# Kernel optimization log

Measured on AMD Instinct MI355X. Metric: run time of the kernel, lower is better.

## Reference

```python
import jax, jax.numpy as jnp
import numpy as np

B = 131072
UNITS = 256
INPUT_DIM = 256


def setup_inputs() -> dict:
    key = jax.random.key(0)
    ks = jax.random.split(key, 8)
    x = jax.random.normal(ks[0], (B, INPUT_DIM), dtype=jnp.float32)
    h_prev = jax.random.normal(ks[1], (B, UNITS), dtype=jnp.float32)
    c_prev = jax.random.normal(ks[2], (B, UNITS), dtype=jnp.float32)
    # glorot-like scale for W: fan_in = INPUT_DIM + UNITS, fan_out = 4*UNITS
    scale = jnp.sqrt(2.0 / (INPUT_DIM + UNITS + 4 * UNITS)).astype(jnp.float32)
    W = jax.random.normal(ks[3], (INPUT_DIM + UNITS, 4 * UNITS), dtype=jnp.float32) * scale
    # bias: zeros except forget gate initialized to 1.0
    b = jnp.concatenate([
        jnp.zeros(UNITS, jnp.float32),
        jnp.ones(UNITS, jnp.float32),
        jnp.zeros(UNITS, jnp.float32),
        jnp.zeros(UNITS, jnp.float32),
    ])
    peephole_i = jax.random.normal(ks[4], (UNITS,), dtype=jnp.float32) * 0.05
    peephole_f = jax.random.normal(ks[5], (UNITS,), dtype=jnp.float32) * 0.05
    peephole_o = jax.random.normal(ks[6], (UNITS,), dtype=jnp.float32) * 0.05
    return {
        "x": x, "h_prev": h_prev, "c_prev": c_prev,
        "W": W, "b": b,
        "peephole_i": peephole_i, "peephole_f": peephole_f, "peephole_o": peephole_o,
    }


def reference(x, h_prev, c_prev, W, b, peephole_i, peephole_f, peephole_o):
    combined = jnp.concatenate([x, h_prev], axis=-1)          # [B, INPUT_DIM+UNITS]
    z = combined @ W + b                                      # [B, 4*UNITS]
    i, f, c_hat, o = jnp.split(z, 4, axis=1)                  # each [B, UNITS]
    i = jax.nn.sigmoid(i + peephole_i * c_prev)
    f = jax.nn.sigmoid(f + peephole_f * c_prev)
    o = jax.nn.sigmoid(o + peephole_o * c_prev)
    c_hat = jnp.tanh(c_hat)
    c = f * c_prev + i * c_hat
    h = o * jnp.tanh(c)
    return (h, h, c)  # matches (output, [h, c]) of the Keras cell
```

## Files before the change

### kernel.cpp

```cpp
#include <hip/hip_runtime.h>
#include <hip/hip_bf16.h>
#include <cstdint>

#define NROWS   131072
#define NUNITS  256
#define N4      1024
#define KTOT    512
#define BM      64
#define THREADS 512

typedef float f32x4 __attribute__((ext_vector_type(4)));
typedef short bf16x8 __attribute__((ext_vector_type(8)));

__device__ __forceinline__ short f2bf(float x) {
    unsigned u = __float_as_uint(x);
    u += 0x7FFFu + ((u >> 16) & 1u);
    return (short)(u >> 16);
}

__global__ void convert_W_kernel(const float* __restrict__ W, short* __restrict__ Wws) {
    int i = blockIdx.x * 256 + threadIdx.x;
    int k = i >> 10;
    int c = i & 1023;
    short b = f2bf(W[i]);
    Wws[((size_t)(k >> 5) << 15) + ((size_t)c << 5) + (k & 31)] = b;
}

__global__ void __launch_bounds__(THREADS, 4)
lstm_main_kernel(const float* __restrict__ x, const float* __restrict__ h_prev,
                 const float* __restrict__ c_prev, const float* __restrict__ bias,
                 const float* __restrict__ pi, const float* __restrict__ pf,
                 const float* __restrict__ po, const short* __restrict__ Wws,
                 float* __restrict__ out) {
    __shared__ short Alds[2][BM * 32];

    const int t    = threadIdx.x;
    const int lane = t & 63;
    const int w    = t >> 6;
    const int rt   = blockIdx.x >> 1;
    const int ch   = blockIdx.x & 1;
    const int row0 = rt * BM;

    const int lr = lane & 15;
    const int hi = lane >> 4;

    const int srow = t >> 3;
    const int sh   = t & 7;
    const int sg   = sh >> 1;
    const int shalf= sh & 1;
    const int s_lds = srow * 32 + ((sg ^ ((srow >> 1) & 3)) * 8) + shalf * 4;
    const float* aRowX = x      + (size_t)(row0 + srow) * 256 + sh * 4;
    const float* aRowH = h_prev + (size_t)(row0 + srow) * 256 + sh * 4;

    const int a_rd = lr * 32 + ((hi ^ ((lr >> 1) & 3)) * 8);

    const int ucol = ch * 128 + w * 16 + lr;
    const short* wbase = Wws + (size_t)ucol * 32 + hi * 8;

    f32x4 acc[4][4];
    #pragma unroll
    for (int m = 0; m < 4; ++m)
        #pragma unroll
        for (int g = 0; g < 4; ++g)
            acc[m][g] = (f32x4){0.f, 0.f, 0.f, 0.f};

    auto stage = [&](int kidx, int buf) {
        const float* src = (kidx < 8 ? aRowX : aRowH) + (kidx & 7) * 32;
        float4 av = *(const float4*)src;
        unsigned p0 = ((unsigned)(unsigned short)f2bf(av.y) << 16) | (unsigned short)f2bf(av.x);
        unsigned p1 = ((unsigned)(unsigned short)f2bf(av.w) << 16) | (unsigned short)f2bf(av.z);
        *(uint2*)(&Alds[buf][s_lds]) = make_uint2(p0, p1);
    };

    auto compute = [&](int ks, int buf) {
        const short* wk = wbase + ((size_t)ks << 15);
        bf16x8 bf[4];
        #pragma unroll
        for (int g = 0; g < 4; ++g)
            bf[g] = *(const bf16x8*)(wk + g * 8192);
        bf16x8 af[4];
        #pragma unroll
        for (int m = 0; m < 4; ++m)
            af[m] = *(const bf16x8*)&Alds[buf][a_rd + m * 16 * 32];
        #pragma unroll
        for (int g = 0; g < 4; ++g)
            #pragma unroll
            for (int m = 0; m < 4; ++m)
                acc[m][g] = __builtin_amdgcn_mfma_f32_16x16x32_bf16(af[m], bf[g], acc[m][g], 0, 0, 0);
    };

    stage(0, 0);
    __syncthreads();

    #pragma unroll 1
    for (int ks2 = 0; ks2 < 8; ++ks2) {
        const int k0 = ks2 * 2;
        stage(k0 + 1, 1);
        compute(k0, 0);
        __syncthreads();
        if (ks2 < 7) stage(k0 + 2, 0);
        compute(k0 + 1, 1);
        __syncthreads();
    }

    const size_t HS = (size_t)NROWS * NUNITS;
    const int u = ucol;
    const float bi = bias[u],       bfg = bias[256 + u];
    const float bc = bias[512 + u], bo  = bias[768 + u];
    const float ppi = pi[u], ppf = pf[u], ppo = po[u];
    #pragma unroll
    for (int m = 0; m < 4; ++m) {
        #pragma unroll
        for (int r = 0; r < 4; ++r) {
            const int row = row0 + m * 16 + hi * 4 + r;
            const size_t o = (size_t)row * NUNITS + u;
            const float cp = c_prev[o];
            float zi = acc[m][0][r] + bi  + ppi * cp;
            float zf = acc[m][1][r] + bfg + ppf * cp;
            float zc = acc[m][2][r] + bc;
            float zo = acc[m][3][r] + bo  + ppo * cp;
            float ig = 1.f / (1.f + __expf(-zi));
            float fg = 1.f / (1.f + __expf(-zf));
            float og = 1.f / (1.f + __expf(-zo));
            zc = fminf(fmaxf(zc, -30.f), 30.f);
            float e2 = __expf(2.f * zc);
            float chat = (e2 - 1.f) / (e2 + 1.f);
            float c  = fg * cp + ig * chat;
            float ccl = fminf(fmaxf(c, -30.f), 30.f);
            float e3 = __expf(2.f * ccl);
            float th = (e3 - 1.f) / (e3 + 1.f);
            float h  = og * th;
            out[o]          = h;
            out[HS + o]     = h;
            out[2 * HS + o] = c;
        }
    }
}

extern "C" void kernel_launch(void* const* d_in, const int* in_sizes, int n_in,
                              void* d_out, int out_size, void* d_ws, size_t ws_size,
                              hipStream_t stream) {
    const float* x  = (const float*)d_in[0];
    const float* h  = (const float*)d_in[1];
    const float* c  = (const float*)d_in[2];
    const float* W  = (const float*)d_in[3];
    const float* b  = (const float*)d_in[4];
    const float* pi = (const float*)d_in[5];
    const float* pf = (const float*)d_in[6];
    const float* po = (const float*)d_in[7];
    short* Wws = (short*)d_ws;
    float* out = (float*)d_out;

    hipLaunchKernelGGL(convert_W_kernel, dim3(2048), dim3(256), 0, stream, W, Wws);
    hipLaunchKernelGGL(lstm_main_kernel, dim3(2 * NROWS / BM), dim3(THREADS), 0, stream,
                       x, h, c, b, pi, pf, po, Wws, out);
}
```

Baseline: 334.5 us.

## Switch to 32x32 MFMA, drop LDS staging, pre-convert activations to bf16

Replaces the 16x16x32 MFMA tiling with 32x32x16 MFMAs. Each wave now owns a 32-row by 32-unit tile per gate and reads A fragments directly from global memory, so the LDS double buffer and the barriers are gone. When the workspace is large enough, a separate kernel first converts x and h_prev into a bf16 concatenated matrix, which halves the A read traffic in the main kernel but adds an extra pass that writes and rereads 128MB. The W workspace layout changes to 16-k chunks to match the new MFMA shape.

```diff
diff --git a/kernel.cpp b/kernel.cpp
--- a/kernel.cpp
+++ b/kernel.cpp
@@ -4,12 +4,12 @@
 
 #define NROWS   131072
 #define NUNITS  256
-#define N4      1024
 #define KTOT    512
 #define BM      64
 #define THREADS 512
 
-typedef float f32x4 __attribute__((ext_vector_type(4)));
+typedef float f32x16 __attribute__((ext_vector_type(16)));
+typedef float f32x4  __attribute__((ext_vector_type(4)));
 typedef short bf16x8 __attribute__((ext_vector_type(8)));
 
 __device__ __forceinline__ short f2bf(float x) {
@@ -22,118 +22,112 @@
     int i = blockIdx.x * 256 + threadIdx.x;
     int k = i >> 10;
     int c = i & 1023;
-    short b = f2bf(W[i]);
-    Wws[((size_t)(k >> 5) << 15) + ((size_t)c << 5) + (k & 31)] = b;
+    Wws[((size_t)(k >> 4) << 14) + ((size_t)c << 4) + (k & 15)] = f2bf(W[i]);
 }
 
+__global__ void convert_A_kernel(const float* __restrict__ x, const float* __restrict__ h,
+                                 short* __restrict__ Aws) {
+    int i = blockIdx.x * 256 + threadIdx.x;
+    int row = i >> 6;
+    int c   = (i & 63) * 4;
+    float4 xv = *(const float4*)(x + (size_t)row * 256 + c);
+    float4 hv = *(const float4*)(h + (size_t)row * 256 + c);
+    short xs[4] = {f2bf(xv.x), f2bf(xv.y), f2bf(xv.z), f2bf(xv.w)};
+    short hs[4] = {f2bf(hv.x), f2bf(hv.y), f2bf(hv.z), f2bf(hv.w)};
+    *(uint2*)(Aws + (size_t)row * 512 + c)       = *(uint2*)xs;
+    *(uint2*)(Aws + (size_t)row * 512 + 256 + c) = *(uint2*)hs;
+}
+
+template<bool PRE>
 __global__ void __launch_bounds__(THREADS, 4)
 lstm_main_kernel(const float* __restrict__ x, const float* __restrict__ h_prev,
                  const float* __restrict__ c_prev, const float* __restrict__ bias,
                  const float* __restrict__ pi, const float* __restrict__ pf,
                  const float* __restrict__ po, const short* __restrict__ Wws,
-                 float* __restrict__ out) {
-    __shared__ short Alds[2][BM * 32];
-
+                 const short* __restrict__ Aws, float* __restrict__ out) {
     const int t    = threadIdx.x;
     const int lane = t & 63;
     const int w    = t >> 6;
+    const int mg   = w >> 2;
+    const int cs   = w & 3;
     const int rt   = blockIdx.x >> 1;
     const int ch   = blockIdx.x & 1;
-    const int row0 = rt * BM;
+    const int l5   = lane & 31;
+    const int k8   = lane >> 5;
 
-    const int lr = lane & 15;
-    const int hi = lane >> 4;
+    const int row  = rt * BM + mg * 32 + l5;
+    const int u    = ch * 128 + cs * 32 + l5;
 
-    const int srow = t >> 3;
-    const int sh   = t & 7;
-    const int sg   = sh >> 1;
-    const int shalf= sh & 1;
-    const int s_lds = srow * 32 + ((sg ^ ((srow >> 1) & 3)) * 8) + shalf * 4;
-    const float* aRowX = x      + (size_t)(row0 + srow) * 256 + sh * 4;
-    const float* aRowH = h_prev + (size_t)(row0 + srow) * 256 + sh * 4;
+    f32x16 acc[4];
+    #pragma unroll
+    for (int g = 0; g < 4; ++g)
+        acc[g] = (f32x16){0.f,0.f,0.f,0.f,0.f,0.f,0.f,0.f,0.f,0.f,0.f,0.f,0.f,0.f,0.f,0.f};
 
-    const int a_rd = lr * 32 + ((hi ^ ((lr >> 1) & 3)) * 8);
+    const short* wbase = Wws + ((size_t)u << 4) + k8 * 8;
+    const short* abase = PRE ? (Aws + (size_t)row * 512 + k8 * 8) : nullptr;
+    const float* xrow  = x      + (size_t)row * 256;
+    const float* hrow  = h_prev + (size_t)row * 256;
 
-    const int ucol = ch * 128 + w * 16 + lr;
-    const short* wbase = Wws + (size_t)ucol * 32 + hi * 8;
-
-    f32x4 acc[4][4];
-    #pragma unroll
-    for (int m = 0; m < 4; ++m)
+    #pragma unroll 2
+    for (int it = 0; it < 16; ++it) {
+        const int k0 = it * 32;
+        bf16x8 A0, A1;
+        if (PRE) {
+            A0 = *(const bf16x8*)(abase + k0);
+            A1 = *(const bf16x8*)(abase + k0 + 16);
+        } else {
+            const int ka = k0 + k8 * 8;
+            const int kb = ka + 16;
+            const float* sa = (ka < 256) ? (xrow + ka) : (hrow + ka - 256);
+            const float* sb = (kb < 256) ? (xrow + kb) : (hrow + kb - 256);
+            float4 va0 = *(const float4*)sa, va1 = *(const float4*)(sa + 4);
+            float4 vb0 = *(const float4*)sb, vb1 = *(const float4*)(sb + 4);
+            short a0[8] = {f2bf(va0.x), f2bf(va0.y), f2bf(va0.z), f2bf(va0.w),
+                           f2bf(va1.x), f2bf(va1.y), f2bf(va1.z), f2bf(va1.w)};
+            short a1[8] = {f2bf(vb0.x), f2bf(vb0.y), f2bf(vb0.z), f2bf(vb0.w),
+                           f2bf(vb1.x), f2bf(vb1.y), f2bf(vb1.z), f2bf(vb1.w)};
+            A0 = *(bf16x8*)a0;
+            A1 = *(bf16x8*)a1;
+        }
+        const short* wk0 = wbase + ((size_t)(2 * it) << 14);
+        const short* wk1 = wk0 + 16384;
         #pragma unroll
-        for (int g = 0; g < 4; ++g)
-            acc[m][g] = (f32x4){0.f, 0.f, 0.f, 0.f};
-
-    auto stage = [&](int kidx, int buf) {
-        const float* src = (kidx < 8 ? aRowX : aRowH) + (kidx & 7) * 32;
-        float4 av = *(const float4*)src;
-        unsigned p0 = ((unsigned)(unsigned short)f2bf(av.y) << 16) | (unsigned short)f2bf(av.x);
-        unsigned p1 = ((unsigned)(unsigned short)f2bf(av.w) << 16) | (unsigned short)f2bf(av.z);
-        *(uint2*)(&Alds[buf][s_lds]) = make_uint2(p0, p1);
-    };
-
-    auto compute = [&](int ks, int buf) {
-        const short* wk = wbase + ((size_t)ks << 15);
-        bf16x8 bf[4];
-        #pragma unroll
-        for (int g = 0; g < 4; ++g)
-            bf[g] = *(const bf16x8*)(wk + g * 8192);
-        bf16x8 af[4];
-        #pragma unroll
-        for (int m = 0; m < 4; ++m)
-            af[m] = *(const bf16x8*)&Alds[buf][a_rd + m * 16 * 32];
-        #pragma unroll
-        for (int g = 0; g < 4; ++g)
-            #pragma unroll
-            for (int m = 0; m < 4; ++m)
-                acc[m][g] = __builtin_amdgcn_mfma_f32_16x16x32_bf16(af[m], bf[g], acc[m][g], 0, 0, 0);
-    };
-
-    stage(0, 0);
-    __syncthreads();
-
-    #pragma unroll 1
-    for (int ks2 = 0; ks2 < 8; ++ks2) {
-        const int k0 = ks2 * 2;
-        stage(k0 + 1, 1);
-        compute(k0, 0);
-        __syncthreads();
-        if (ks2 < 7) stage(k0 + 2, 0);
-        compute(k0 + 1, 1);
-        __syncthreads();
+        for (int g = 0; g < 4; ++g) {
+            bf16x8 B0 = *(const bf16x8*)(wk0 + g * 4096);
+            bf16x8 B1 = *(const bf16x8*)(wk1 + g * 4096);
+            acc[g] = __builtin_amdgcn_mfma_f32_32x32x16_bf16(A0, B0, acc[g], 0, 0, 0);
+            acc[g] = __builtin_amdgcn_mfma_f32_32x32x16_bf16(A1, B1, acc[g], 0, 0, 0);
+        }
     }
 
     const size_t HS = (size_t)NROWS * NUNITS;
-    const int u = ucol;
     const float bi = bias[u],       bfg = bias[256 + u];
     const float bc = bias[512 + u], bo  = bias[768 + u];
     const float ppi = pi[u], ppf = pf[u], ppo = po[u];
+    const int rowbase = rt * BM + mg * 32 + 4 * k8;
     #pragma unroll
-    for (int m = 0; m < 4; ++m) {
-        #pragma unroll
-        for (int r = 0; r < 4; ++r) {
-            const int row = row0 + m * 16 + hi * 4 + r;
-            const size_t o = (size_t)row * NUNITS + u;
-            const float cp = c_prev[o];
-            float zi = acc[m][0][r] + bi  + ppi * cp;
-            float zf = acc[m][1][r] + bfg + ppf * cp;
-            float zc = acc[m][2][r] + bc;
-            float zo = acc[m][3][r] + bo  + ppo * cp;
-            float ig = 1.f / (1.f + __expf(-zi));
-            float fg = 1.f / (1.f + __expf(-zf));
-            float og = 1.f / (1.f + __expf(-zo));
-            zc = fminf(fmaxf(zc, -30.f), 30.f);
-            float e2 = __expf(2.f * zc);
-            float chat = (e2 - 1.f) / (e2 + 1.f);
-            float c  = fg * cp + ig * chat;
-            float ccl = fminf(fmaxf(c, -30.f), 30.f);
-            float e3 = __expf(2.f * ccl);
-            float th = (e3 - 1.f) / (e3 + 1.f);
-            float h  = og * th;
-            out[o]          = h;
-            out[HS + o]     = h;
-            out[2 * HS + o] = c;
-        }
+    for (int r = 0; r < 16; ++r) {
+        const int rr = rowbase + (r & 3) + 8 * (r >> 2);
+        const size_t o = (size_t)rr * NUNITS + u;
+        const float cp = c_prev[o];
+        float zi = acc[0][r] + bi  + ppi * cp;
+        float zf = acc[1][r] + bfg + ppf * cp;
+        float zc = acc[2][r] + bc;
+        float zo = acc[3][r] + bo  + ppo * cp;
+        float ig = 1.f / (1.f + __expf(-zi));
+        float fg = 1.f / (1.f + __expf(-zf));
+        float og = 1.f / (1.f + __expf(-zo));
+        zc = fminf(fmaxf(zc, -30.f), 30.f);
+        float e2 = __expf(2.f * zc);
+        float chat = (e2 - 1.f) / (e2 + 1.f);
+        float c  = fg * cp + ig * chat;
+        float ccl = fminf(fmaxf(c, -30.f), 30.f);
+        float e3 = __expf(2.f * ccl);
+        float th = (e3 - 1.f) / (e3 + 1.f);
+        float h  = og * th;
+        out[o]          = h;
+        out[HS + o]     = h;
+        out[2 * HS + o] = c;
     }
 }
 
@@ -148,10 +142,22 @@
     const float* pi = (const float*)d_in[5];
     const float* pf = (const float*)d_in[6];
     const float* po = (const float*)d_in[7];
-    short* Wws = (short*)d_ws;
     float* out = (float*)d_out;
 
-    hipLaunchKernelGGL(convert_W_kernel, dim3(2048), dim3(256), 0, stream, W, Wws);
-    hipLaunchKernelGGL(lstm_main_kernel, dim3(2 * NROWS / BM), dim3(THREADS), 0, stream,
-                       x, h, c, b, pi, pf, po, Wws, out);
+    const size_t aws_bytes = (size_t)NROWS * KTOT * 2;
+    const size_t wws_bytes = (size_t)KTOT * 1024 * 2;
+
+    if (ws_size >= aws_bytes + wws_bytes) {
+        short* Aws = (short*)d_ws;
+        short* Wws = (short*)((char*)d_ws + aws_bytes);
+        hipLaunchKernelGGL(convert_A_kernel, dim3(32768), dim3(256), 0, stream, x, h, Aws);
+        hipLaunchKernelGGL(convert_W_kernel, dim3(2048), dim3(256), 0, stream, W, Wws);
+        hipLaunchKernelGGL((lstm_main_kernel<true>), dim3(2 * NROWS / BM), dim3(THREADS), 0,
+                           stream, x, h, c, b, pi, pf, po, Wws, Aws, out);
+    } else {
+        short* Wws = (short*)d_ws;
+        hipLaunchKernelGGL(convert_W_kernel, dim3(2048), dim3(256), 0, stream, W, Wws);
+        hipLaunchKernelGGL((lstm_main_kernel<false>), dim3(2 * NROWS / BM), dim3(THREADS), 0,
+                           stream, x, h, c, b, pi, pf, po, Wws, nullptr, out);
+    }
 }
```

New measurement: 496.1 us. 48.3% more time.

## Prefetch W fragments and A loads a step ahead; swizzle block order

Applied to the files above, without the earlier changes.

The K loop is restructured so the global loads for the next step's A tile and W fragments are issued before the current step's MFMAs. The converted A data is written to LDS only after the compute, so load latency is hidden behind math. __syncthreads is replaced by a custom barrier that waits only on LDS counters. Block indices are also remapped with a stride-8 swizzle that changes which row tiles run concurrently, presumably for cache or XCD locality. Holding the extra B fragments in registers raises register pressure under the 4-blocks launch bound.

```diff
diff --git a/kernel.cpp b/kernel.cpp
--- a/kernel.cpp
+++ b/kernel.cpp
@@ -4,12 +4,11 @@
 
 #define NROWS   131072
 #define NUNITS  256
-#define N4      1024
 #define KTOT    512
 #define BM      64
 #define THREADS 512
 
-typedef float f32x4 __attribute__((ext_vector_type(4)));
+typedef float f32x4  __attribute__((ext_vector_type(4)));
 typedef short bf16x8 __attribute__((ext_vector_type(8)));
 
 __device__ __forceinline__ short f2bf(float x) {
@@ -18,12 +17,14 @@
     return (short)(u >> 16);
 }
 
+#define BAR() do { asm volatile("s_waitcnt lgkmcnt(0)" ::: "memory"); \
+                   __builtin_amdgcn_s_barrier(); } while (0)
+
 __global__ void convert_W_kernel(const float* __restrict__ W, short* __restrict__ Wws) {
     int i = blockIdx.x * 256 + threadIdx.x;
     int k = i >> 10;
     int c = i & 1023;
-    short b = f2bf(W[i]);
-    Wws[((size_t)(k >> 5) << 15) + ((size_t)c << 5) + (k & 31)] = b;
+    Wws[((size_t)(k >> 5) << 15) + ((size_t)c << 5) + (k & 31)] = f2bf(W[i]);
 }
 
 __global__ void __launch_bounds__(THREADS, 4)
@@ -34,20 +35,22 @@
                  float* __restrict__ out) {
     __shared__ short Alds[2][BM * 32];
 
+    const int bid = blockIdx.x;
+    const int swz = (bid & 7) * 512 + (bid >> 3);
+    const int rt  = swz >> 1;
+    const int ch  = swz & 1;
+    const int row0 = rt * BM;
+
     const int t    = threadIdx.x;
     const int lane = t & 63;
     const int w    = t >> 6;
-    const int rt   = blockIdx.x >> 1;
-    const int ch   = blockIdx.x & 1;
-    const int row0 = rt * BM;
+    const int lr   = lane & 15;
+    const int hi   = lane >> 4;
 
-    const int lr = lane & 15;
-    const int hi = lane >> 4;
-
-    const int srow = t >> 3;
-    const int sh   = t & 7;
-    const int sg   = sh >> 1;
-    const int shalf= sh & 1;
+    const int srow  = t >> 3;
+    const int sh    = t & 7;
+    const int sg    = sh >> 1;
+    const int shalf = sh & 1;
     const int s_lds = srow * 32 + ((sg ^ ((srow >> 1) & 3)) * 8) + shalf * 4;
     const float* aRowX = x      + (size_t)(row0 + srow) * 256 + sh * 4;
     const float* aRowH = h_prev + (size_t)(row0 + srow) * 256 + sh * 4;
@@ -55,7 +58,7 @@
     const int a_rd = lr * 32 + ((hi ^ ((lr >> 1) & 3)) * 8);
 
     const int ucol = ch * 128 + w * 16 + lr;
-    const short* wbase = Wws + (size_t)ucol * 32 + hi * 8;
+    const short* wbase = Wws + ((size_t)ucol << 5) + hi * 8;
 
     f32x4 acc[4][4];
     #pragma unroll
@@ -64,20 +67,23 @@
         for (int g = 0; g < 4; ++g)
             acc[m][g] = (f32x4){0.f, 0.f, 0.f, 0.f};
 
-    auto stage = [&](int kidx, int buf) {
-        const float* src = (kidx < 8 ? aRowX : aRowH) + (kidx & 7) * 32;
-        float4 av = *(const float4*)src;
+    bf16x8 Bcur[4], Bnext[4];
+
+    auto loadA4 = [&](int kidx) -> float4 {
+        return *(const float4*)((kidx < 8 ? aRowX : aRowH) + (kidx & 7) * 32);
+    };
+    auto writeA = [&](float4 av, int buf) {
         unsigned p0 = ((unsigned)(unsigned short)f2bf(av.y) << 16) | (unsigned short)f2bf(av.x);
         unsigned p1 = ((unsigned)(unsigned short)f2bf(av.w) << 16) | (unsigned short)f2bf(av.z);
         *(uint2*)(&Alds[buf][s_lds]) = make_uint2(p0, p1);
     };
-
-    auto compute = [&](int ks, int buf) {
+    auto loadB = [&](int ks, bf16x8* B) {
         const short* wk = wbase + ((size_t)ks << 15);
-        bf16x8 bf[4];
         #pragma unroll
         for (int g = 0; g < 4; ++g)
-            bf[g] = *(const bf16x8*)(wk + g * 8192);
+            B[g] = *(const bf16x8*)(wk + g * 8192);
+    };
+    auto compute = [&](const bf16x8* B, int buf) {
         bf16x8 af[4];
         #pragma unroll
         for (int m = 0; m < 4; ++m)
@@ -86,21 +92,41 @@
         for (int g = 0; g < 4; ++g)
             #pragma unroll
             for (int m = 0; m < 4; ++m)
-                acc[m][g] = __builtin_amdgcn_mfma_f32_16x16x32_bf16(af[m], bf[g], acc[m][g], 0, 0, 0);
+                acc[m][g] = __builtin_amdgcn_mfma_f32_16x16x32_bf16(af[m], B[g], acc[m][g], 0, 0, 0);
     };
 
-    stage(0, 0);
-    __syncthreads();
+    {
+        float4 av0 = loadA4(0);
+        loadB(0, Bcur);
+        writeA(av0, 0);
+        BAR();
+    }
 
     #pragma unroll 1
-    for (int ks2 = 0; ks2 < 8; ++ks2) {
-        const int k0 = ks2 * 2;
-        stage(k0 + 1, 1);
-        compute(k0, 0);
-        __syncthreads();
-        if (ks2 < 7) stage(k0 + 2, 0);
-        compute(k0 + 1, 1);
-        __syncthreads();
+    for (int it2 = 0; it2 < 7; ++it2) {
+        const int k0 = 2 * it2;
+        {
+            float4 av = loadA4(k0 + 1);
+            loadB(k0 + 1, Bnext);
+            compute(Bcur, 0);
+            writeA(av, 1);
+            BAR();
+        }
+        {
+            float4 av = loadA4(k0 + 2);
+            loadB(k0 + 2, Bcur);
+            compute(Bnext, 1);
+            writeA(av, 0);
+            BAR();
+        }
+    }
+    {
+        float4 av = loadA4(15);
+        loadB(15, Bnext);
+        compute(Bcur, 0);
+        writeA(av, 1);
+        BAR();
+        compute(Bnext, 1);
     }
 
     const size_t HS = (size_t)NROWS * NUNITS;
```

Result: slower. 347.6 us (+3.9%).

## Pre-convert activations to bf16 and stream A/B tiles via global_load_lds triple buffering

Applied to the files above, without the earlier changes.

Adds a conversion pass that writes x and h_prev as a bf16 workspace matrix alongside the W conversion. The main kernel then loads swizzled A and W tiles straight into LDS with global_load_lds DMA, using a three-stage buffer ring and vmcnt waits in place of register staging and direct global W loads. Blocks become 128 rows by 64 units, with block index swizzling for locality. The goal is to remove per-iteration conversion and uncoalesced W global loads from the GEMM loop. The cost is an extra full pass writing and re-reading a 128MB bf16 activation copy.

```diff
diff --git a/kernel.cpp b/kernel.cpp
--- a/kernel.cpp
+++ b/kernel.cpp
@@ -1,15 +1,13 @@
 #include <hip/hip_runtime.h>
-#include <hip/hip_bf16.h>
 #include <cstdint>
 
 #define NROWS   131072
 #define NUNITS  256
-#define N4      1024
 #define KTOT    512
-#define BM      64
+#define BM      128
 #define THREADS 512
 
-typedef float f32x4 __attribute__((ext_vector_type(4)));
+typedef float f32x4  __attribute__((ext_vector_type(4)));
 typedef short bf16x8 __attribute__((ext_vector_type(8)));
 
 __device__ __forceinline__ short f2bf(float x) {
@@ -18,44 +16,60 @@
     return (short)(u >> 16);
 }
 
-__global__ void convert_W_kernel(const float* __restrict__ W, short* __restrict__ Wws) {
-    int i = blockIdx.x * 256 + threadIdx.x;
-    int k = i >> 10;
-    int c = i & 1023;
-    short b = f2bf(W[i]);
-    Wws[((size_t)(k >> 5) << 15) + ((size_t)c << 5) + (k & 31)] = b;
+__global__ void convert_kernel(const float* __restrict__ x, const float* __restrict__ h,
+                               const float* __restrict__ W,
+                               short* __restrict__ Aws, short* __restrict__ Wws) {
+    int b = blockIdx.x;
+    if (b < 32768) {
+        int i = b * 256 + threadIdx.x;
+        int row = i >> 6;
+        int c   = (i & 63) * 4;
+        float4 xv = *(const float4*)(x + (size_t)row * 256 + c);
+        float4 hv = *(const float4*)(h + (size_t)row * 256 + c);
+        short xs[4] = {f2bf(xv.x), f2bf(xv.y), f2bf(xv.z), f2bf(xv.w)};
+        short hs[4] = {f2bf(hv.x), f2bf(hv.y), f2bf(hv.z), f2bf(hv.w)};
+        *(uint2*)(Aws + (size_t)row * 512 + c)       = *(uint2*)xs;
+        *(uint2*)(Aws + (size_t)row * 512 + 256 + c) = *(uint2*)hs;
+    } else {
+        int i = (b - 32768) * 256 + threadIdx.x;
+        int k = i >> 10;
+        int c = i & 1023;
+        Wws[((size_t)(k >> 5) << 15) + ((size_t)c << 5) + (k & 31)] = f2bf(W[i]);
+    }
 }
 
 __global__ void __launch_bounds__(THREADS, 4)
-lstm_main_kernel(const float* __restrict__ x, const float* __restrict__ h_prev,
-                 const float* __restrict__ c_prev, const float* __restrict__ bias,
+lstm_main_kernel(const float* __restrict__ c_prev, const float* __restrict__ bias,
                  const float* __restrict__ pi, const float* __restrict__ pf,
-                 const float* __restrict__ po, const short* __restrict__ Wws,
-                 float* __restrict__ out) {
-    __shared__ short Alds[2][BM * 32];
+                 const float* __restrict__ po, const short* __restrict__ Aws,
+                 const short* __restrict__ Wws, float* __restrict__ out) {
+    __shared__ short lds[3][12288];
+
+    const int bid = blockIdx.x;
+    const int swz = (bid & 7) * 512 + (bid >> 3);
+    const int ut  = swz & 3;
+    const int rt  = swz >> 2;
+    const int row0 = rt * BM;
 
     const int t    = threadIdx.x;
     const int lane = t & 63;
     const int w    = t >> 6;
-    const int rt   = blockIdx.x >> 1;
-    const int ch   = blockIdx.x & 1;
-    const int row0 = rt * BM;
+    const int lr   = lane & 15;
+    const int hi   = lane >> 4;
+    const int rh   = w >> 2;
+    const int q    = w & 3;
 
-    const int lr = lane & 15;
-    const int hi = lane >> 4;
+    const int arow = t >> 2, ags = t & 3;
+    const short* srcA = Aws + (size_t)(row0 + arow) * 512 + ((ags ^ (arow & 3)) * 8);
+    const int G1 = t + 512;
+    const int g0 = t >> 8,  u0 = (t >> 2) & 63,  s0 = t & 3;
+    const int g1 = G1 >> 8, u1 = (G1 >> 2) & 63, s1 = G1 & 3;
+    const short* srcB0 = Wws + (size_t)(g0 * 256 + ut * 64 + u0) * 32 + ((s0 ^ (u0 & 3)) * 8);
+    const short* srcB1 = Wws + (size_t)(g1 * 256 + ut * 64 + u1) * 32 + ((s1 ^ (u1 & 3)) * 8);
 
-    const int srow = t >> 3;
-    const int sh   = t & 7;
-    const int sg   = sh >> 1;
-    const int shalf= sh & 1;
-    const int s_lds = srow * 32 + ((sg ^ ((srow >> 1) & 3)) * 8) + shalf * 4;
-    const float* aRowX = x      + (size_t)(row0 + srow) * 256 + sh * 4;
-    const float* aRowH = h_prev + (size_t)(row0 + srow) * 256 + sh * 4;
-
-    const int a_rd = lr * 32 + ((hi ^ ((lr >> 1) & 3)) * 8);
-
-    const int ucol = ch * 128 + w * 16 + lr;
-    const short* wbase = Wws + (size_t)ucol * 32 + hi * 8;
+    const int sw8  = (hi ^ (lr & 3)) * 8;
+    const int aoff = (rh * 64 + lr) * 32 + sw8;
+    const int boff = 4096 + (q * 16 + lr) * 32 + sw8;
 
     f32x4 acc[4][4];
     #pragma unroll
@@ -64,47 +78,54 @@
         for (int g = 0; g < 4; ++g)
             acc[m][g] = (f32x4){0.f, 0.f, 0.f, 0.f};
 
-    auto stage = [&](int kidx, int buf) {
-        const float* src = (kidx < 8 ? aRowX : aRowH) + (kidx & 7) * 32;
-        float4 av = *(const float4*)src;
-        unsigned p0 = ((unsigned)(unsigned short)f2bf(av.y) << 16) | (unsigned short)f2bf(av.x);
-        unsigned p1 = ((unsigned)(unsigned short)f2bf(av.w) << 16) | (unsigned short)f2bf(av.z);
-        *(uint2*)(&Alds[buf][s_lds]) = make_uint2(p0, p1);
+    auto issueDMA = [&](int ks, int buf) {
+        short* dst = &lds[buf][0];
+        __builtin_amdgcn_global_load_lds(
+            (const __attribute__((address_space(1))) uint32_t*)(const void*)(srcA + ks * 32),
+            (__attribute__((address_space(3))) uint32_t*)(void*)(dst + w * 512), 16, 0, 0);
+        __builtin_amdgcn_global_load_lds(
+            (const __attribute__((address_space(1))) uint32_t*)(const void*)(srcB0 + (size_t)ks * 32768),
+            (__attribute__((address_space(3))) uint32_t*)(void*)(dst + 4096 + w * 512), 16, 0, 0);
+        __builtin_amdgcn_global_load_lds(
+            (const __attribute__((address_space(1))) uint32_t*)(const void*)(srcB1 + (size_t)ks * 32768),
+            (__attribute__((address_space(3))) uint32_t*)(void*)(dst + 8192 + w * 512), 16, 0, 0);
     };
 
-    auto compute = [&](int ks, int buf) {
-        const short* wk = wbase + ((size_t)ks << 15);
-        bf16x8 bf[4];
+    auto compute = [&](int buf) {
+        const short* L = &lds[buf][0];
+        bf16x8 af[4], bfr[4];
+        #pragma unroll
+        for (int m = 0; m < 4; ++m)
+            af[m] = *(const bf16x8*)&L[aoff + m * 512];
         #pragma unroll
         for (int g = 0; g < 4; ++g)
-            bf[g] = *(const bf16x8*)(wk + g * 8192);
-        bf16x8 af[4];
-        #pragma unroll
-        for (int m = 0; m < 4; ++m)
-            af[m] = *(const bf16x8*)&Alds[buf][a_rd + m * 16 * 32];
+            bfr[g] = *(const bf16x8*)&L[boff + g * 2048];
         #pragma unroll
         for (int g = 0; g < 4; ++g)
             #pragma unroll
             for (int m = 0; m < 4; ++m)
-                acc[m][g] = __builtin_amdgcn_mfma_f32_16x16x32_bf16(af[m], bf[g], acc[m][g], 0, 0, 0);
+                acc[m][g] = __builtin_amdgcn_mfma_f32_16x16x32_bf16(af[m], bfr[g], acc[m][g], 0, 0, 0);
     };
 
-    stage(0, 0);
-    __syncthreads();
+    issueDMA(0, 0);
+    issueDMA(1, 1);
 
+    int cur = 0;
     #pragma unroll 1
-    for (int ks2 = 0; ks2 < 8; ++ks2) {
-        const int k0 = ks2 * 2;
-        stage(k0 + 1, 1);
-        compute(k0, 0);
-        __syncthreads();
-        if (ks2 < 7) stage(k0 + 2, 0);
-        compute(k0 + 1, 1);
-        __syncthreads();
+    for (int p = 0; p < 16; ++p) {
+        if (p < 15) { asm volatile("s_waitcnt vmcnt(3)" ::: "memory"); }
+        else        { asm volatile("s_waitcnt vmcnt(0)" ::: "memory"); }
+        __builtin_amdgcn_s_barrier();
+        if (p < 14) {
+            int nb = cur + 2; if (nb >= 3) nb -= 3;
+            issueDMA(p + 2, nb);
+        }
+        compute(cur);
+        if (++cur == 3) cur = 0;
     }
 
     const size_t HS = (size_t)NROWS * NUNITS;
-    const int u = ucol;
+    const int u = ut * 64 + q * 16 + lr;
     const float bi = bias[u],       bfg = bias[256 + u];
     const float bc = bias[512 + u], bo  = bias[768 + u];
     const float ppi = pi[u], ppf = pf[u], ppo = po[u];
@@ -112,7 +133,7 @@
     for (int m = 0; m < 4; ++m) {
         #pragma unroll
         for (int r = 0; r < 4; ++r) {
-            const int row = row0 + m * 16 + hi * 4 + r;
+            const int row = row0 + rh * 64 + m * 16 + hi * 4 + r;
             const size_t o = (size_t)row * NUNITS + u;
             const float cp = c_prev[o];
             float zi = acc[m][0][r] + bi  + ppi * cp;
@@ -148,10 +169,14 @@
     const float* pi = (const float*)d_in[5];
     const float* pf = (const float*)d_in[6];
     const float* po = (const float*)d_in[7];
-    short* Wws = (short*)d_ws;
     float* out = (float*)d_out;
 
-    hipLaunchKernelGGL(convert_W_kernel, dim3(2048), dim3(256), 0, stream, W, Wws);
-    hipLaunchKernelGGL(lstm_main_kernel, dim3(2 * NROWS / BM), dim3(THREADS), 0, stream,
-                       x, h, c, b, pi, pf, po, Wws, out);
+    const size_t aws_bytes = (size_t)NROWS * KTOT * 2;
+    short* Aws = (short*)d_ws;
+    short* Wws = (short*)((char*)d_ws + aws_bytes);
+
+    hipLaunchKernelGGL(convert_kernel, dim3(32768 + 2048), dim3(256), 0, stream,
+                       x, h, W, Aws, Wws);
+    hipLaunchKernelGGL(lstm_main_kernel, dim3(NROWS / BM * 4), dim3(THREADS), 0, stream,
+                       c, b, pi, pf, po, Aws, Wws, out);
 }
```

Result: faster. 322.1 us (-3.7%).
